# Optimization experiments

Hardware: AMD Instinct MI355X
Metric: run time of the kernel (lower is better)

The kernel has to match this reference:

```python
import jax, jax.numpy as jnp
import numpy as np

COMMITMENT_COST = 0.25
NUM_EMBEDDINGS = 8192
EMBEDDING_DIM = 256


def setup_inputs() -> dict:
    key = jax.random.key(0)
    k1, k2 = jax.random.split(key)
    inputs = jax.random.normal(k1, (32, 256, EMBEDDING_DIM), dtype=jnp.float32)
    codebook = jax.random.normal(k2, (NUM_EMBEDDINGS, EMBEDDING_DIM), dtype=jnp.float32)
    # match nn.Embedding init: N(0,1) then L2-normalize rows
    codebook = codebook / jnp.linalg.norm(codebook, axis=1, keepdims=True)
    return {"inputs": inputs, "codebook": codebook}


def reference(inputs, codebook):
    B, K, D = inputs.shape
    flat = inputs.reshape(-1, D).astype(jnp.float32)  # [N, D], N = B*K
    N = flat.shape[0]

    distances = (
        jnp.sum(flat * flat, axis=1, keepdims=True)
        + jnp.sum(codebook * codebook, axis=1)
        - 2.0 * flat @ codebook.T
    )
    indices = jnp.argmin(distances, axis=1)  # [N]

    # codebook lookup (equivalent to one-hot @ codebook)
    quantized = codebook[indices].reshape(B, K, D)

    e_latent_loss = jnp.mean((jax.lax.stop_gradient(quantized) - inputs) ** 2)
    q_latent_loss = jnp.mean((quantized - jax.lax.stop_gradient(inputs)) ** 2)
    loss = q_latent_loss + COMMITMENT_COST * e_latent_loss

    # straight-through estimator
    quantized_ste = inputs + jax.lax.stop_gradient(quantized - inputs)

    # perplexity from codebook usage histogram (== mean of one-hot encodings)
    counts = jnp.zeros((NUM_EMBEDDINGS,), dtype=jnp.float32).at[indices].add(1.0)
    avg_probs = counts / N
    perplexity = jnp.exp(-jnp.sum(avg_probs * jnp.log(avg_probs + 1e-10)))

    return quantized_ste, loss, perplexity
```

## Files before the change

### kernel.cpp

```cpp
#include <hip/hip_runtime.h>
#include <math.h>

#define NTOK 8192
#define NEMB 8192
#define DIM  256

typedef _Float16 f16x8 __attribute__((ext_vector_type(8)));
typedef _Float16 f16x4 __attribute__((ext_vector_type(4)));
typedef float    f32x4 __attribute__((ext_vector_type(4)));

__global__ __launch_bounds__(256) void convert_kernel(
        const float* __restrict__ X, const float* __restrict__ C,
        _Float16* __restrict__ Xh, _Float16* __restrict__ Ch,
        float* __restrict__ cnorm, float* __restrict__ xnorm,
        unsigned long long* __restrict__ keys, int* __restrict__ counts) {
    const bool isC = (blockIdx.y != 0);
    if (isC && blockIdx.x < 8) {
        ((int4*)counts)[blockIdx.x * 256 + threadIdx.x] = make_int4(0, 0, 0, 0);
    }
    if (!isC && blockIdx.x < 8) {
        int4 ff = make_int4(-1, -1, -1, -1);
        ((int4*)keys)[blockIdx.x * 512 + threadIdx.x * 2]     = ff;
        ((int4*)keys)[blockIdx.x * 512 + threadIdx.x * 2 + 1] = ff;
    }
    const float* src = isC ? C : X;
    _Float16* dst = isC ? Ch : Xh;
    size_t t = (size_t)blockIdx.x * 256 + threadIdx.x;
    float4 x = *(const float4*)&src[t * 4];
    f16x4 h;
    h[0] = (_Float16)x.x; h[1] = (_Float16)x.y;
    h[2] = (_Float16)x.z; h[3] = (_Float16)x.w;
    *(f16x4*)&dst[t * 4] = h;
    float s = x.x * x.x + x.y * x.y + x.z * x.z + x.w * x.w;
    #pragma unroll
    for (int off = 32; off >= 1; off >>= 1) s += __shfl_xor(s, off);
    if ((threadIdx.x & 63) == 0) {
        if (isC) cnorm[t >> 6] = s; else xnorm[t >> 6] = s;
    }
}

__device__ __forceinline__ int swz(int row) { return (row + (row >> 2)) & 3; }

template<int N>
__device__ __forceinline__ void wait_vmcnt() {
    asm volatile("s_waitcnt vmcnt(%0)" :: "n"(N) : "memory");
}

__device__ __forceinline__ void stage_k32(
        const _Float16* __restrict__ Ag, const _Float16* __restrict__ Bg,
        _Float16* bufA, _Float16* bufB, int t) {
    #pragma unroll
    for (int c = 0; c < 2; ++c) {
        int gr  = c * 512 + t;
        int row = gr >> 2;
        int kg  = (gr & 3) ^ swz(row);
        __builtin_amdgcn_global_load_lds(
            (const __attribute__((address_space(1))) void*)(Ag + (size_t)row * DIM + kg * 8),
            (__attribute__((address_space(3))) void*)(bufA + (size_t)gr * 8), 16, 0, 0);
    }
    {
        int gr  = t;
        int row = gr >> 2;
        int kg  = (gr & 3) ^ swz(row);
        __builtin_amdgcn_global_load_lds(
            (const __attribute__((address_space(1))) void*)(Bg + (size_t)row * DIM + kg * 8),
            (__attribute__((address_space(3))) void*)(bufB + (size_t)gr * 8), 16, 0, 0);
    }
}

__device__ __forceinline__ void compute_k32(
        const _Float16* Abuf, const _Float16* Bbuf, f32x4 (&acc)[4][4],
        int wm, int wn, int lrow, int g) {
    f16x8 af[4], bf_[4];
    #pragma unroll
    for (int i = 0; i < 4; ++i) {
        int row = wm + i * 16 + lrow;
        af[i] = *(const f16x8*)&Abuf[(row * 4 + (g ^ swz(row))) * 8];
    }
    #pragma unroll
    for (int j = 0; j < 4; ++j) {
        int row = wn + j * 16 + lrow;
        bf_[j] = *(const f16x8*)&Bbuf[(row * 4 + (g ^ swz(row))) * 8];
    }
    __builtin_amdgcn_s_setprio(1);
    #pragma unroll
    for (int i = 0; i < 4; ++i)
        #pragma unroll
        for (int j = 0; j < 4; ++j)
            acc[i][j] = __builtin_amdgcn_mfma_f32_16x16x32_f16(
                af[i], bf_[j], acc[i][j], 0, 0, 0);
    __builtin_amdgcn_s_setprio(0);
}

__global__ __launch_bounds__(512, 4) void mfma_argmin_kernel(
        const _Float16* __restrict__ Xh, const _Float16* __restrict__ Ch,
        const float* __restrict__ cnorm,
        unsigned long long* __restrict__ keys) {
    __shared__ __align__(16) _Float16 lds[36864];
    _Float16* const ldsB = lds + 24576;

    const int t = threadIdx.x;
    const int wid = t >> 6, lane = t & 63;
    const int tb0 = blockIdx.x * 128;
    const int cb0 = blockIdx.y * 256;
    const int wm = (wid >> 1) * 64;
    const int wn = (wid & 1) * 64;
    const int lrow = lane & 15;
    const int g = lane >> 4;

    f32x4 acc[4][4];
    #pragma unroll
    for (int a = 0; a < 4; ++a)
        #pragma unroll
        for (int b = 0; b < 4; ++b) acc[a][b] = (f32x4)0.0f;

    const _Float16* Ag = Ch + (size_t)cb0 * DIM;
    const _Float16* Bg = Xh + (size_t)tb0 * DIM;

    stage_k32(Ag,      Bg,      lds,        ldsB,        t);
    stage_k32(Ag + 32, Bg + 32, lds + 8192, ldsB + 4096, t);

#define PHASE(P, WAITN)                                                       \
    do {                                                                      \
        wait_vmcnt<WAITN>();                                                  \
        __builtin_amdgcn_s_barrier();                                         \
        __builtin_amdgcn_sched_barrier(0);                                    \
        if ((P) + 2 < 8)                                                      \
            stage_k32(Ag + ((P) + 2) * 32, Bg + ((P) + 2) * 32,               \
                      lds + (((P) + 2) % 3) * 8192,                           \
                      ldsB + (((P) + 2) % 3) * 4096, t);                      \
        compute_k32(lds + ((P) % 3) * 8192, ldsB + ((P) % 3) * 4096,          \
                    acc, wm, wn, lrow, g);                                    \
        __builtin_amdgcn_sched_barrier(0);                                    \
    } while (0)

    PHASE(0, 3); PHASE(1, 3); PHASE(2, 3); PHASE(3, 3);
    PHASE(4, 3); PHASE(5, 3); PHASE(6, 3); PHASE(7, 0);
#undef PHASE

    float cn[16];
    #pragma unroll
    for (int tm = 0; tm < 4; ++tm)
        #pragma unroll
        for (int reg = 0; reg < 4; ++reg)
            cn[tm * 4 + reg] = cnorm[cb0 + wm + tm * 16 + g * 4 + reg];

    float* cmb_v = (float*)lds;
    int*   cmb_i = (int*)((float*)lds + 512);

    #pragma unroll
    for (int tn = 0; tn < 4; ++tn) {
        float bv = 1e30f; int bi = 0x7fffffff;
        #pragma unroll
        for (int tm = 0; tm < 4; ++tm) {
            #pragma unroll
            for (int reg = 0; reg < 4; ++reg) {
                float d = fmaf(-2.0f, acc[tm][tn][reg], cn[tm * 4 + reg]);
                int code = cb0 + wm + tm * 16 + g * 4 + reg;
                if (d < bv) { bv = d; bi = code; }
            }
        }
        #pragma unroll
        for (int off = 16; off <= 32; off <<= 1) {
            float ov = __shfl_xor(bv, off);
            int   oi = __shfl_xor(bi, off);
            if (ov < bv || (ov == bv && oi < bi)) { bv = ov; bi = oi; }
        }
        if (g == 0) {
            int tl = wn + tn * 16 + lrow;
            cmb_v[tl * 4 + (wid >> 1)] = bv;
            cmb_i[tl * 4 + (wid >> 1)] = bi;
        }
    }
    __syncthreads();
    if (t < 128) {
        float bv = cmb_v[t * 4]; int bi = cmb_i[t * 4];
        #pragma unroll
        for (int w = 1; w < 4; ++w) {
            float ov = cmb_v[t * 4 + w];
            int   oi = cmb_i[t * 4 + w];
            if (ov < bv || (ov == bv && oi < bi)) { bv = ov; bi = oi; }
        }
        unsigned long long key =
            ((unsigned long long)__builtin_bit_cast(unsigned, bv + 64.0f) << 32)
            | (unsigned)bi;
        atomicMin(&keys[tb0 + t], key);
    }
}

__global__ __launch_bounds__(256) void gather_kernel(
        const float* __restrict__ C, const unsigned long long* __restrict__ keys,
        const float* __restrict__ xnorm, int* __restrict__ counts,
        float* __restrict__ out, float* __restrict__ psum) {
    __shared__ int idx_lds[32];
    const int m0 = blockIdx.x * 32;
    const int t = threadIdx.x;
    if (t < 32) {
        unsigned long long k = keys[m0 + t];
        int bi  = (int)(unsigned)k;
        float d = __builtin_bit_cast(float, (unsigned)(k >> 32)) - 64.0f;
        idx_lds[t] = bi;
        atomicAdd(&counts[bi], 1);
        float lt = d + xnorm[m0 + t];
        #pragma unroll
        for (int off = 1; off < 32; off <<= 1) lt += __shfl_xor(lt, off);
        if (t == 0) psum[blockIdx.x] = lt;
    }
    __syncthreads();
    const int wid = t >> 6, lane = t & 63;
    #pragma unroll
    for (int r = 0; r < 8; ++r) {
        int token = m0 + wid * 8 + r;
        int e = idx_lds[wid * 8 + r];
        float4 q = *(const float4*)&C[(size_t)e * DIM + lane * 4];
        *(float4*)&out[(size_t)token * DIM + lane * 4] = q;
    }
}

__global__ __launch_bounds__(1024) void finalize_kernel(
        const int* __restrict__ counts, const float* __restrict__ psum,
        float* __restrict__ out) {
    const int t = threadIdx.x;
    double local = 0.0;
    #pragma unroll
    for (int i = 0; i < 8; ++i) {
        int e = t + i * 1024;
        float p = (float)counts[e] * (1.0f / (float)NTOK);
        local += (double)(p * logf(p + 1e-10f));
    }
    float ls = (t < 256) ? psum[t] : 0.0f;
    #pragma unroll
    for (int off = 32; off >= 1; off >>= 1) {
        local += __shfl_xor(local, off);
        ls    += __shfl_xor(ls, off);
    }
    __shared__ double she[16];
    __shared__ float  shs[16];
    int lane = t & 63, wid = t >> 6;
    if (lane == 0) { she[wid] = local; shs[wid] = ls; }
    __syncthreads();
    if (t == 0) {
        double ent = 0.0; float ssq = 0.0f;
        #pragma unroll
        for (int w = 0; w < 16; ++w) { ent += she[w]; ssq += shs[w]; }
        out[(size_t)NTOK * DIM]     = 1.25f * ssq / (float)((size_t)NTOK * DIM);
        out[(size_t)NTOK * DIM + 1] = expf((float)(-ent));
    }
}

extern "C" void kernel_launch(void* const* d_in, const int* in_sizes, int n_in,
                              void* d_out, int out_size, void* d_ws, size_t ws_size,
                              hipStream_t stream) {
    const float* X = (const float*)d_in[0];
    const float* C = (const float*)d_in[1];
    float* out = (float*)d_out;

    char* ws = (char*)d_ws;
    size_t o = 0;
    _Float16* Xh = (_Float16*)(ws + o); o += (size_t)NTOK * DIM * 2;
    _Float16* Ch = (_Float16*)(ws + o); o += (size_t)NEMB * DIM * 2;
    float* cnorm = (float*)(ws + o); o += (size_t)NEMB * 4;
    float* xnorm = (float*)(ws + o); o += (size_t)NTOK * 4;
    unsigned long long* keys = (unsigned long long*)(ws + o); o += (size_t)NTOK * 8;
    int* counts  = (int*)(ws + o);   o += (size_t)NEMB * 4;
    float* psum  = (float*)(ws + o);

    convert_kernel<<<dim3(NTOK * DIM / 4 / 256, 2), 256, 0, stream>>>(
        X, C, Xh, Ch, cnorm, xnorm, keys, counts);
    mfma_argmin_kernel<<<dim3(NTOK / 128, NEMB / 256), 512, 0, stream>>>(
        Xh, Ch, cnorm, keys);
    gather_kernel<<<256, 256, 0, stream>>>(
        C, keys, xnorm, counts, out, psum);
    finalize_kernel<<<1, 1024, 0, stream>>>(counts, psum, out);
}
```

Baseline: 117.2 us.

## Fuse gather and finalize into argmin kernel via last-block atomic counters

Removes the separate gather and finalize launches. The last of the 32 codebook-tile blocks for each token tile now does the index gather, histogram counting and loss partial sum. A global counter then picks the final block, which computes the perplexity and loss. This saves two kernel launches and their boundaries, at the cost of extra fences, atomics and a serialized tail inside the main kernel.

```diff
diff --git a/kernel.cpp b/kernel.cpp
--- a/kernel.cpp
+++ b/kernel.cpp
@@ -13,10 +13,14 @@
         const float* __restrict__ X, const float* __restrict__ C,
         _Float16* __restrict__ Xh, _Float16* __restrict__ Ch,
         float* __restrict__ cnorm, float* __restrict__ xnorm,
-        unsigned long long* __restrict__ keys, int* __restrict__ counts) {
+        unsigned long long* __restrict__ keys, int* __restrict__ counts,
+        unsigned* __restrict__ ctrl) {
     const bool isC = (blockIdx.y != 0);
     if (isC && blockIdx.x < 8) {
         ((int4*)counts)[blockIdx.x * 256 + threadIdx.x] = make_int4(0, 0, 0, 0);
+    }
+    if (isC && blockIdx.x == 8 && threadIdx.x < 65) {
+        ctrl[threadIdx.x] = 0;
     }
     if (!isC && blockIdx.x < 8) {
         int4 ff = make_int4(-1, -1, -1, -1);
@@ -95,9 +99,17 @@
 __global__ __launch_bounds__(512, 4) void mfma_argmin_kernel(
         const _Float16* __restrict__ Xh, const _Float16* __restrict__ Ch,
         const float* __restrict__ cnorm,
-        unsigned long long* __restrict__ keys) {
+        unsigned long long* __restrict__ keys,
+        const float* __restrict__ C, const float* __restrict__ xnorm,
+        int* __restrict__ counts, float* __restrict__ out,
+        float* __restrict__ psum, unsigned* __restrict__ ctrl) {
     __shared__ __align__(16) _Float16 lds[36864];
     _Float16* const ldsB = lds + 24576;
+    __shared__ int   sidx[128];
+    __shared__ float spart[8];
+    __shared__ double sdd[8];
+    __shared__ float  sls[8];
+    __shared__ int sflag;
 
     const int t = threadIdx.x;
     const int wid = t >> 6, lane = t & 63;
@@ -186,65 +198,68 @@
             | (unsigned)bi;
         atomicMin(&keys[tb0 + t], key);
     }
-}
-
-__global__ __launch_bounds__(256) void gather_kernel(
-        const float* __restrict__ C, const unsigned long long* __restrict__ keys,
-        const float* __restrict__ xnorm, int* __restrict__ counts,
-        float* __restrict__ out, float* __restrict__ psum) {
-    __shared__ int idx_lds[32];
-    const int m0 = blockIdx.x * 32;
-    const int t = threadIdx.x;
-    if (t < 32) {
-        unsigned long long k = keys[m0 + t];
-        int bi  = (int)(unsigned)k;
-        float d = __builtin_bit_cast(float, (unsigned)(k >> 32)) - 64.0f;
-        idx_lds[t] = bi;
-        atomicAdd(&counts[bi], 1);
-        float lt = d + xnorm[m0 + t];
-        #pragma unroll
-        for (int off = 1; off < 32; off <<= 1) lt += __shfl_xor(lt, off);
-        if (t == 0) psum[blockIdx.x] = lt;
-    }
-    __syncthreads();
-    const int wid = t >> 6, lane = t & 63;
-    #pragma unroll
-    for (int r = 0; r < 8; ++r) {
-        int token = m0 + wid * 8 + r;
-        int e = idx_lds[wid * 8 + r];
-        float4 q = *(const float4*)&C[(size_t)e * DIM + lane * 4];
-        *(float4*)&out[(size_t)token * DIM + lane * 4] = q;
-    }
-}
-
-__global__ __launch_bounds__(1024) void finalize_kernel(
-        const int* __restrict__ counts, const float* __restrict__ psum,
-        float* __restrict__ out) {
-    const int t = threadIdx.x;
-    double local = 0.0;
-    #pragma unroll
-    for (int i = 0; i < 8; ++i) {
-        int e = t + i * 1024;
-        float p = (float)counts[e] * (1.0f / (float)NTOK);
-        local += (double)(p * logf(p + 1e-10f));
-    }
-    float ls = (t < 256) ? psum[t] : 0.0f;
-    #pragma unroll
-    for (int off = 32; off >= 1; off >>= 1) {
-        local += __shfl_xor(local, off);
-        ls    += __shfl_xor(ls, off);
-    }
-    __shared__ double she[16];
-    __shared__ float  shs[16];
-    int lane = t & 63, wid = t >> 6;
-    if (lane == 0) { she[wid] = local; shs[wid] = ls; }
+
     __syncthreads();
     if (t == 0) {
-        double ent = 0.0; float ssq = 0.0f;
-        #pragma unroll
-        for (int w = 0; w < 16; ++w) { ent += she[w]; ssq += shs[w]; }
-        out[(size_t)NTOK * DIM]     = 1.25f * ssq / (float)((size_t)NTOK * DIM);
-        out[(size_t)NTOK * DIM + 1] = expf((float)(-ent));
+        __threadfence();
+        unsigned o = atomicAdd(&ctrl[blockIdx.x], 1u);
+        sflag = (o == 31u) ? 1 : 0;
+    }
+    __syncthreads();
+    if (sflag) {
+        __threadfence();
+        if (t < 128) {
+            unsigned long long k = keys[tb0 + t];
+            int bi  = (int)(unsigned)k;
+            float d = __builtin_bit_cast(float, (unsigned)(k >> 32)) - 64.0f;
+            sidx[t] = bi;
+            atomicAdd(&counts[bi], 1);
+            float lt = d + xnorm[tb0 + t];
+            #pragma unroll
+            for (int off = 32; off >= 1; off >>= 1) lt += __shfl_xor(lt, off);
+            if ((t & 63) == 0) spart[t >> 6] = lt;
+        }
+        __syncthreads();
+        #pragma unroll
+        for (int r = 0; r < 16; ++r) {
+            int tl = wid * 16 + r;
+            int e  = sidx[tl];
+            float4 q = *(const float4*)&C[(size_t)e * DIM + lane * 4];
+            *(float4*)&out[(size_t)(tb0 + tl) * DIM + lane * 4] = q;
+        }
+        if (t == 0) psum[blockIdx.x] = spart[0] + spart[1];
+        __syncthreads();
+        if (t == 0) {
+            __threadfence();
+            unsigned o2 = atomicAdd(&ctrl[64], 1u);
+            sflag = (o2 == 63u) ? 2 : 1;
+        }
+        __syncthreads();
+        if (sflag == 2) {
+            __threadfence();
+            double local = 0.0;
+            #pragma unroll
+            for (int i = 0; i < 16; ++i) {
+                int e = t + i * 512;
+                float p = (float)counts[e] * (1.0f / (float)NTOK);
+                local += (double)(p * logf(p + 1e-10f));
+            }
+            float ls = (t < 64) ? psum[t] : 0.0f;
+            #pragma unroll
+            for (int off = 32; off >= 1; off >>= 1) {
+                local += __shfl_xor(local, off);
+                ls    += __shfl_xor(ls, off);
+            }
+            if (lane == 0) { sdd[wid] = local; sls[wid] = ls; }
+            __syncthreads();
+            if (t == 0) {
+                double ent = 0.0; float ssq = 0.0f;
+                #pragma unroll
+                for (int w = 0; w < 8; ++w) { ent += sdd[w]; ssq += sls[w]; }
+                out[(size_t)NTOK * DIM]     = 1.25f * ssq / (float)((size_t)NTOK * DIM);
+                out[(size_t)NTOK * DIM + 1] = expf((float)(-ent));
+            }
+        }
     }
 }
 
@@ -263,13 +278,11 @@
     float* xnorm = (float*)(ws + o); o += (size_t)NTOK * 4;
     unsigned long long* keys = (unsigned long long*)(ws + o); o += (size_t)NTOK * 8;
     int* counts  = (int*)(ws + o);   o += (size_t)NEMB * 4;
-    float* psum  = (float*)(ws + o);
+    float* psum  = (float*)(ws + o); o += (size_t)64 * 4;
+    unsigned* ctrl = (unsigned*)(ws + o);
 
     convert_kernel<<<dim3(NTOK * DIM / 4 / 256, 2), 256, 0, stream>>>(
-        X, C, Xh, Ch, cnorm, xnorm, keys, counts);
+        X, C, Xh, Ch, cnorm, xnorm, keys, counts, ctrl);
     mfma_argmin_kernel<<<dim3(NTOK / 128, NEMB / 256), 512, 0, stream>>>(
-        Xh, Ch, cnorm, keys);
-    gather_kernel<<<256, 256, 0, stream>>>(
-        C, keys, xnorm, counts, out, psum);
-    finalize_kernel<<<1, 1024, 0, stream>>>(counts, psum, out);
-}
+        Xh, Ch, cnorm, keys, C, xnorm, counts, out, psum, ctrl);
+}
```

Measured after the change: 153.4 us. +30.9%, slower.
